# Optimization experiments

Measured on AMD Instinct MI355X. Metric: run time of the kernel, lower is better.

The kernel has to match this reference:

```python
import jax, jax.numpy as jnp
import numpy as np

HEADS, BS, HALO = 8, 8, 3
WIN = BS + 2 * HALO  # 14


def setup_inputs() -> dict:
    key = jax.random.key(0)
    k1, k2, k3, k4 = jax.random.split(key, 4)
    B, C, H, W = 16, 256, 64, 64
    dim_out_qk, dim_out_v = 256, 256
    std = C ** (-0.5)
    x = jax.random.normal(k1, (B, C, H, W), jnp.float32)
    Wq = jax.random.normal(k2, (dim_out_qk, C), jnp.float32) * std
    Wkv = jax.random.normal(k3, (dim_out_qk + dim_out_v, C), jnp.float32) * std
    pos_bias = jax.random.normal(k4, (HEADS, BS * BS, WIN * WIN), jnp.float32) * 0.02
    return {"x": x, "Wq": Wq, "Wkv": Wkv, "pos_bias": pos_bias}


def reference(x, Wq, Wkv, pos_bias):
    B, C, H, W = x.shape
    dhqk = Wq.shape[0] // HEADS            # 32
    dhv = Wkv.shape[0] // HEADS - dhqk     # 32
    scale = dhqk ** (-0.5)
    nhb, nwb = H // BS, W // BS
    nb = nhb * nwb

    xl = jnp.transpose(x, (0, 2, 3, 1))    # [B, H, W, C]

    # queries: [B, heads, nb, bs^2, dhqk] (row-major within block)
    q = xl @ Wq.T
    q = q.reshape(B, nhb, BS, nwb, BS, HEADS, dhqk)
    q = q.transpose(0, 5, 1, 3, 2, 4, 6).reshape(B, HEADS, nb, BS * BS, dhqk)

    # keys/values via overlapping halo windows (zero-padded unfold)
    kv = xl @ Wkv.T                                       # [B, H, W, dim_kv]
    kv = jnp.pad(kv, ((0, 0), (HALO, HALO), (HALO, HALO), (0, 0)))
    ridx = (jnp.arange(nhb) * BS)[:, None] + jnp.arange(WIN)[None, :]
    cidx = (jnp.arange(nwb) * BS)[:, None] + jnp.arange(WIN)[None, :]
    kv = kv[:, ridx]
    kv = kv[:, :, :, cidx]
    kv = kv.transpose(0, 1, 3, 2, 4, 5).reshape(B, nb, WIN * WIN, HEADS, dhqk + dhv)
    k = kv[..., :dhqk]
    v = kv[..., dhqk:]

    attn = jnp.einsum('bhnqd,bnkhd->bhnqk', q, k) * scale + pos_bias[None, :, None]
    attn = jax.nn.softmax(attn, axis=-1)
    out = jnp.einsum('bhnqk,bnkhd->bhnqd', attn, v)       # [B, heads, nb, bs^2, dhv]

    out = out.reshape(B, HEADS, nhb, nwb, BS, BS, dhv)
    out = out.transpose(0, 1, 6, 2, 4, 3, 5).reshape(B, HEADS * dhv, H, W)
    return out
```

## Files before the change

kernel.cpp:

```cpp
#include <hip/hip_runtime.h>
#include <hip/hip_bf16.h>
#include <stdint.h>

#define HEADS 8
#define WIN 14
#define NPOS 196
#define NPAD 224
#define NB 16
#define NC 256
#define NH 64
#define NW 64
#define NP 4096
#define NKV 512
#define NOC 768

typedef __bf16 bf16_t;
typedef bf16_t bf16x8 __attribute__((ext_vector_type(8)));
typedef float f32x4 __attribute__((ext_vector_type(4)));

union Frag {
  uint4 u4;
  bf16x8 b8;
  ushort us[8];
};

__device__ __forceinline__ ushort f2bf(float f) {
  bf16_t h = (bf16_t)f;
  return __builtin_bit_cast(ushort, h);
}
__device__ __forceinline__ bf16x8 load_bf8(const float* __restrict__ p) {
  float4 a = *reinterpret_cast<const float4*>(p);
  float4 b = *reinterpret_cast<const float4*>(p + 4);
  bf16x8 r;
  r[0] = (bf16_t)a.x; r[1] = (bf16_t)a.y; r[2] = (bf16_t)a.z; r[3] = (bf16_t)a.w;
  r[4] = (bf16_t)b.x; r[5] = (bf16_t)b.y; r[6] = (bf16_t)b.z; r[7] = (bf16_t)b.w;
  return r;
}

__device__ __forceinline__ void gload_lds16(const ushort* g, ushort* l) {
#if __has_builtin(__builtin_amdgcn_global_load_lds)
  __builtin_amdgcn_global_load_lds(
      (const __attribute__((address_space(1))) unsigned int*)(const void*)g,
      (__attribute__((address_space(3))) unsigned int*)(void*)l, 16, 0, 0);
#else
  *reinterpret_cast<uint4*>(l) = *reinterpret_cast<const uint4*>(g);
#endif
}

__device__ ushort g_wb[NOC * NC];
__device__ float g_pb2[HEADS * 4 * 14 * 256];

__global__ __launch_bounds__(256) void k_prep(const float* __restrict__ wq,
                                              const float* __restrict__ wkv,
                                              const float* __restrict__ pb) {
  const int wg = blockIdx.x;
  const int tid = threadIdx.x;
  if (wg < 96) {
    int idx = (wg * 256 + tid) * 8;
    int oc = idx >> 8, c = idx & 255;
    const float* src = (oc < 256) ? (wq + (size_t)oc * NC + c)
                                  : (wkv + (size_t)(oc - 256) * NC + c);
    Frag v;
    v.b8 = load_bf8(src);
    *reinterpret_cast<uint4*>(g_wb + idx) = v.u4;
  } else {
    int idx2 = wg - 96;
    int h = idx2 / 56;
    int rem = idx2 - h * 56;
    int w = rem / 14;
    int nt = rem - w * 14;
    int lane = tid >> 2, r = tid & 3;
    int quad = lane >> 4, lc = lane & 15;
    int q = w * 16 + lc;
    int key = nt * 16 + quad * 4 + r;
    float v = -100000.0f;
    if (key < NPOS)
      v = pb[((size_t)(h * 64 + q)) * NPOS + key] * 1.4426950408889634f;
    g_pb2[(size_t)idx2 * 256 + tid] = v;
  }
}

__global__ __launch_bounds__(256) void k_xt(const float* __restrict__ x,
                                            ushort* __restrict__ xt) {
  __shared__ __align__(16) ushort ls[64][66];
  const int b = blockIdx.z, p0 = blockIdx.x * 64, c0 = blockIdx.y * 64;
  const int by8 = blockIdx.y * 8;
  const int tid = threadIdx.x;
  #pragma unroll
  for (int it = 0; it < 4; ++it) {
    int i = it * 256 + tid;
    int c = i >> 4, ps = (i & 15) * 4;
    float4 v = *reinterpret_cast<const float4*>(x + ((size_t)(b * NC + c0 + c)) * NP + p0 + ps);
    ls[ps + 0][c] = f2bf(v.x);
    ls[ps + 1][c] = f2bf(v.y);
    ls[ps + 2][c] = f2bf(v.z);
    ls[ps + 3][c] = f2bf(v.w);
  }
  __syncthreads();
  #pragma unroll
  for (int it = 0; it < 2; ++it) {
    int i = it * 256 + tid;
    int p = i >> 3, gl = i & 7;
    Frag o;
    #pragma unroll
    for (int j = 0; j < 8; ++j) o.us[j] = ls[p][gl * 8 + j];
    int gph = by8 + (gl ^ (p & 7));
    *reinterpret_cast<uint4*>(xt + ((size_t)(b * NP) + p0 + p) * NC + gph * 8) = o.u4;
  }
}

__global__ __launch_bounds__(256, 2) void k_proj2(const ushort* __restrict__ xt,
                                                  ushort* __restrict__ qkv) {
  __shared__ __align__(16) ushort As[128 * 256];
  const int row0 = blockIdx.x * 128;
  const int n0 = blockIdx.y * 256;
  const int tid = threadIdx.x, lane = tid & 63, wid = tid >> 6;
  const int quad = lane >> 4, lc = lane & 15;
  const ushort* gs = xt + (size_t)row0 * NC;
  #pragma unroll
  for (int it = 0; it < 16; ++it) {
    int f = it * 256 + tid;
    gload_lds16(gs + (size_t)f * 8, As + f * 8);
  }
  __syncthreads();
  const int wm = (wid & 1) * 64, wn = (wid >> 1) * 128;
  f32x4 acc[4][8] = {};
  #pragma unroll
  for (int ks = 0; ks < 8; ++ks) {
    const int k0 = ks * 32 + quad * 8;
    Frag a[4];
    #pragma unroll
    for (int mt = 0; mt < 4; ++mt) {
      int row = wm + mt * 16 + lc;
      int gk = (ks * 4 + quad) ^ (lc & 7);
      a[mt].u4 = *reinterpret_cast<const uint4*>(&As[row * 256 + gk * 8]);
    }
    #pragma unroll
    for (int ng = 0; ng < 2; ++ng) {
      Frag bb[4];
      #pragma unroll
      for (int j = 0; j < 4; ++j) {
        int oc = n0 + wn + (ng * 4 + j) * 16 + lc;
        bb[j].u4 = *reinterpret_cast<const uint4*>(g_wb + (size_t)oc * NC + k0);
      }
      #pragma unroll
      for (int mt = 0; mt < 4; ++mt)
        #pragma unroll
        for (int j = 0; j < 4; ++j)
          acc[mt][ng * 4 + j] = __builtin_amdgcn_mfma_f32_16x16x32_bf16(
              a[mt].b8, bb[j].b8, acc[mt][ng * 4 + j], 0, 0, 0);
    }
  }
  __syncthreads();
  #pragma unroll
  for (int mt = 0; mt < 4; ++mt)
    #pragma unroll
    for (int nn = 0; nn < 8; ++nn) {
      int row = wm + mt * 16 + quad * 4;
      #pragma unroll
      for (int r = 0; r < 4; ++r) {
        int rr = row + r;
        int col = wn + nn * 16 + lc;
        As[rr * 256 + (((col >> 3) ^ (rr & 7)) * 8) + (col & 7)] = f2bf(acc[mt][nn][r]);
      }
    }
  __syncthreads();
  #pragma unroll
  for (int it = 0; it < 16; ++it) {
    int i = it * 256 + tid;
    int r = i >> 5, g = i & 31;
    uint4 u = *reinterpret_cast<const uint4*>(&As[r * 256 + ((g ^ (r & 7)) * 8)]);
    *reinterpret_cast<uint4*>(qkv + ((size_t)(row0 + r)) * NOC + n0 + g * 8) = u;
  }
}

__global__ __launch_bounds__(256) void k_attn_f2(const ushort* __restrict__ qkv,
                                                 float* __restrict__ out) {
  __shared__ __align__(16) ushort ksh[NPAD][40];
  __shared__ __align__(16) ushort vth[32][232];
  float (*osh)[33] = reinterpret_cast<float(*)[33]>(&ksh[0][0]);
  const int orig = blockIdx.x;
  const int wgid = (orig & 7) * 1024 + (orig >> 3);
  const int h = wgid & 7;
  const int blk = (wgid >> 3) & 63;
  const int b = wgid >> 9;
  const int by = blk >> 3, bx = blk & 7;
  const int tid = threadIdx.x, lane = tid & 63, w = tid >> 6;
  const int quad = lane >> 4, lc = lane & 15;

  Frag aq;
  {
    int q = w * 16 + lc;
    int py = by * 8 + (q >> 3), px = bx * 8 + (q & 7);
    aq.u4 = *reinterpret_cast<const uint4*>(
        qkv + ((size_t)(b * NP + py * NW + px)) * NOC + h * 32 + quad * 8);
  }

  #pragma unroll
  for (int it = 0; it < 7; ++it) {
    int i = it * 256 + tid;
    int pos = i >> 3, seg = i & 7;
    Frag v;
    v.u4 = make_uint4(0u, 0u, 0u, 0u);
    if (pos < NPOS) {
      int wy = pos / WIN;
      int wx = pos - wy * WIN;
      int yq = by * 8 - 3 + wy, xx = bx * 8 - 3 + wx;
      if ((unsigned)yq < (unsigned)NH && (unsigned)xx < (unsigned)NW)
        v.u4 = *reinterpret_cast<const uint4*>(
            qkv + ((size_t)(b * NP + yq * NW + xx)) * NOC + 256 + h * 64 + seg * 8);
    }
    if (seg < 4) {
      *reinterpret_cast<uint4*>(&ksh[pos][seg * 8]) = v.u4;
    } else {
      int d0 = (seg - 4) * 8;
      int cp = pos ^ ((seg - 4) << 3);
      #pragma unroll
      for (int j = 0; j < 8; ++j) vth[d0 + j][cp] = v.us[j];
    }
  }
  __syncthreads();

  f32x4 s[14];
  __builtin_amdgcn_s_setprio(1);
  #pragma unroll
  for (int nt = 0; nt < 14; ++nt) {
    Frag bk;
    bk.u4 = *reinterpret_cast<const uint4*>(&ksh[nt * 16 + lc][quad * 8]);
    f32x4 z = {0.f, 0.f, 0.f, 0.f};
    s[nt] = __builtin_amdgcn_mfma_f32_16x16x32_bf16(bk.b8, aq.b8, z, 0, 0, 0);
  }
  __builtin_amdgcn_s_setprio(0);

  const float ck = 0.17677669529663687f * 1.4426950408889634f;
  const float* __restrict__ pbw = g_pb2 + (size_t)((h * 4 + w) * 14) * 256;
  float lsum = 0.f;
  #pragma unroll
  for (int nt = 0; nt < 14; ++nt) {
    float4 bv4 = *reinterpret_cast<const float4*>(pbw + nt * 256 + lane * 4);
    #pragma unroll
    for (int r = 0; r < 4; ++r) {
      float p = exp2f(s[nt][r] * ck + (&bv4.x)[r]);
      s[nt][r] = p;
      lsum += p;
    }
  }

  f32x4 o[2] = {};
  #pragma unroll
  for (int kt = 0; kt < 7; ++kt) {
    Frag pa;
    #pragma unroll
    for (int j = 0; j < 8; ++j)
      pa.us[j] = f2bf(s[2 * kt + (j >> 2)][j & 3]);
    #pragma unroll
    for (int t = 0; t < 2; ++t) {
      int d = t * 16 + lc;
      int xr = ((d >> 3) & 3) << 3;
      int c0 = (kt * 32 + quad * 4) ^ xr;
      int c1 = (kt * 32 + 16 + quad * 4) ^ xr;
      Frag bv;
      *reinterpret_cast<uint2*>(&bv.us[0]) = *reinterpret_cast<const uint2*>(&vth[d][c0]);
      *reinterpret_cast<uint2*>(&bv.us[4]) = *reinterpret_cast<const uint2*>(&vth[d][c1]);
      o[t] = __builtin_amdgcn_mfma_f32_16x16x32_bf16(pa.b8, bv.b8, o[t], 0, 0, 0);
    }
  }

  lsum += __shfl_xor(lsum, 16);
  lsum += __shfl_xor(lsum, 32);
  float rl = 1.0f / lsum;
  float rinv[4];
  #pragma unroll
  for (int r = 0; r < 4; ++r)
    rinv[r] = __shfl(rl, (lane & 48) + quad * 4 + r);

  __syncthreads();
  #pragma unroll
  for (int t = 0; t < 2; ++t)
    #pragma unroll
    for (int r = 0; r < 4; ++r)
      osh[w * 16 + quad * 4 + r][t * 16 + lc] = o[t][r] * rinv[r];
  __syncthreads();

  {
    int d = tid >> 3, yy = tid & 7;
    float4 o0, o1;
    o0.x = osh[yy * 8 + 0][d]; o0.y = osh[yy * 8 + 1][d];
    o0.z = osh[yy * 8 + 2][d]; o0.w = osh[yy * 8 + 3][d];
    o1.x = osh[yy * 8 + 4][d]; o1.y = osh[yy * 8 + 5][d];
    o1.z = osh[yy * 8 + 6][d]; o1.w = osh[yy * 8 + 7][d];
    float* op = out + ((size_t)(b * NC + h * 32 + d) * NH + by * 8 + yy) * NW + bx * 8;
    *reinterpret_cast<float4*>(op) = o0;
    *reinterpret_cast<float4*>(op + 4) = o1;
  }
}

__global__ __launch_bounds__(256) void k_proj_r4(const float* __restrict__ x,
                                                 const float* __restrict__ wq,
                                                 const float* __restrict__ wkv,
                                                 ushort* __restrict__ qkv) {
  __shared__ __align__(16) ushort As[64][264];
  const int b = blockIdx.z, y = blockIdx.x;
  const int n0 = blockIdx.y * 256;
  const int tid = threadIdx.x, lane = tid & 63, wid = tid >> 6;
  const int quad = lane >> 4, lc = lane & 15;
  #pragma unroll
  for (int it = 0; it < 16; ++it) {
    int i = it * 256 + tid;
    int c = i >> 4, xs = (i & 15) * 4;
    float4 v = *reinterpret_cast<const float4*>(x + ((size_t)(b * NC + c)) * NP + y * NW + xs);
    #pragma unroll
    for (int j = 0; j < 4; ++j) {
      int row = xs + j;
      float f = (j == 0) ? v.x : (j == 1) ? v.y : (j == 2) ? v.z : v.w;
      As[row][c ^ ((((row >> 2) & 3)) << 3)] = f2bf(f);
    }
  }
  __syncthreads();
  const int wm = (wid & 1) * 32, wn = (wid >> 1) * 128;
  const int swz = ((lc >> 2) & 3) << 3;
  f32x4 acc[2][8] = {};
  #pragma unroll
  for (int ks = 0; ks < 8; ++ks) {
    const int k0 = ks * 32 + quad * 8;
    Frag a0, a1;
    a0.u4 = *reinterpret_cast<const uint4*>(&As[wm + lc][k0 ^ swz]);
    a1.u4 = *reinterpret_cast<const uint4*>(&As[wm + 16 + lc][k0 ^ swz]);
    #pragma unroll
    for (int nh = 0; nh < 2; ++nh) {
      bf16x8 bb[4];
      #pragma unroll
      for (int nt = 0; nt < 4; ++nt) {
        int oc = n0 + wn + nh * 64 + nt * 16 + lc;
        const float* wp = (oc < 256) ? (wq + (size_t)oc * NC) : (wkv + (size_t)(oc - 256) * NC);
        bb[nt] = load_bf8(wp + k0);
      }
      #pragma unroll
      for (int nt = 0; nt < 4; ++nt) {
        acc[0][nh * 4 + nt] = __builtin_amdgcn_mfma_f32_16x16x32_bf16(a0.b8, bb[nt], acc[0][nh * 4 + nt], 0, 0, 0);
        acc[1][nh * 4 + nt] = __builtin_amdgcn_mfma_f32_16x16x32_bf16(a1.b8, bb[nt], acc[1][nh * 4 + nt], 0, 0, 0);
      }
    }
  }
  __syncthreads();
  #pragma unroll
  for (int mt = 0; mt < 2; ++mt)
    #pragma unroll
    for (int nn = 0; nn < 8; ++nn)
      #pragma unroll
      for (int r = 0; r < 4; ++r)
        As[wm + mt * 16 + quad * 4 + r][wn + nn * 16 + lc] = f2bf(acc[mt][nn][r]);
  __syncthreads();
  #pragma unroll
  for (int v8 = 0; v8 < 8; ++v8) {
    int flat = v8 * 256 + tid;
    int p = flat >> 5, seg = flat & 31;
    uint4 u = *reinterpret_cast<const uint4*>(&As[p][seg * 8]);
    *reinterpret_cast<uint4*>(qkv + ((size_t)(b * NP) + y * NW + p) * NOC + n0 + seg * 8) = u;
  }
}

__global__ __launch_bounds__(256) void k_kv(const float* __restrict__ x,
                                            const float* __restrict__ wkv,
                                            ushort* __restrict__ kvb) {
  __shared__ __align__(16) ushort As[64][264];
  const int b = blockIdx.z;
  const int y = blockIdx.x;
  const int n0 = blockIdx.y * 128;
  const int tid = threadIdx.x;
  const int lane = tid & 63, wid = tid >> 6;
  const int quad = lane >> 4, lc = lane & 15;
  #pragma unroll
  for (int it = 0; it < 16; ++it) {
    int i = it * 256 + tid;
    int c = i >> 4, xs = (i & 15) * 4;
    float4 v = *reinterpret_cast<const float4*>(x + ((size_t)(b * NC + c)) * NP + y * NW + xs);
    As[xs + 0][c] = f2bf(v.x);
    As[xs + 1][c] = f2bf(v.y);
    As[xs + 2][c] = f2bf(v.z);
    As[xs + 3][c] = f2bf(v.w);
  }
  __syncthreads();
  const int wm = (wid & 1) * 32, wn = (wid >> 1) * 64;
  f32x4 acc[2][4] = {};
  #pragma unroll
  for (int ks = 0; ks < 8; ++ks) {
    const int k0 = ks * 32 + quad * 8;
    Frag a[2];
    bf16x8 bb[4];
    #pragma unroll
    for (int mt = 0; mt < 2; ++mt)
      a[mt].u4 = *reinterpret_cast<const uint4*>(&As[wm + mt * 16 + lc][k0]);
    #pragma unroll
    for (int nt = 0; nt < 4; ++nt) {
      int oc = n0 + wn + nt * 16 + lc;
      bb[nt] = load_bf8(wkv + (size_t)oc * NC + k0);
    }
    #pragma unroll
    for (int mt = 0; mt < 2; ++mt)
      #pragma unroll
      for (int nt = 0; nt < 4; ++nt)
        acc[mt][nt] = __builtin_amdgcn_mfma_f32_16x16x32_bf16(a[mt].b8, bb[nt], acc[mt][nt], 0, 0, 0);
  }
  #pragma unroll
  for (int mt = 0; mt < 2; ++mt) {
    #pragma unroll
    for (int r = 0; r < 4; ++r) {
      int pl = wm + mt * 16 + quad * 4 + r;
      #pragma unroll
      for (int nt = 0; nt < 4; ++nt) {
        int oc = n0 + wn + nt * 16 + lc;
        kvb[((size_t)(b * NP + y * NW + pl)) * NKV + oc] = f2bf(acc[mt][nt][r]);
      }
    }
  }
}

__global__ __launch_bounds__(256) void k_attn_v3(const float* __restrict__ x,
                                                 const float* __restrict__ wq,
                                                 const ushort* __restrict__ kvb,
                                                 const float* __restrict__ pbias,
                                                 float* __restrict__ out) {
  __shared__ __align__(16) ushort ksh[NPAD][40];
  __shared__ __align__(16) ushort vth[32][232];
  __shared__ __align__(16) ushort psh[4][16][232];
  __shared__ __align__(16) ushort qsh[4][16][32];
  __shared__ __align__(16) float osh[64][33];
  const int b = blockIdx.z, h = blockIdx.y, blk = blockIdx.x;
  const int by = blk >> 3, bx = blk & 7;
  const int tid = threadIdx.x, lane = tid & 63, w = tid >> 6;
  const int quad = lane >> 4, lc = lane & 15;

  for (int it = 0; it < 7; ++it) {
    int i = it * 256 + tid;
    int pos = i >> 3, seg = i & 7;
    Frag v;
    v.u4 = make_uint4(0u, 0u, 0u, 0u);
    if (pos < NPOS) {
      int wy = pos / WIN;
      int wx = pos - wy * WIN;
      int yq = by * 8 - 3 + wy, xx = bx * 8 - 3 + wx;
      if ((unsigned)yq < (unsigned)NH && (unsigned)xx < (unsigned)NW)
        v.u4 = *reinterpret_cast<const uint4*>(
            kvb + ((size_t)(b * NP + yq * NW + xx)) * NKV + h * 64 + seg * 8);
    }
    if (seg < 4) {
      *reinterpret_cast<uint4*>(&ksh[pos][seg * 8]) = v.u4;
    } else {
      int d0 = (seg - 4) * 8;
      #pragma unroll
      for (int j = 0; j < 8; ++j) vth[d0 + j][pos] = v.us[j];
    }
  }

  f32x4 qacc[2] = {};
  {
    const int q = w * 16 + lc;
    const size_t p = (size_t)(by * 8 + (q >> 3)) * NW + bx * 8 + (q & 7);
    #pragma unroll
    for (int ks = 0; ks < 8; ++ks) {
      const int k0 = ks * 32 + quad * 8;
      Frag ax;
      #pragma unroll
      for (int j = 0; j < 8; ++j)
        ax.us[j] = f2bf(x[((size_t)(b * NC + k0 + j)) * NP + p]);
      bf16x8 bw0 = load_bf8(wq + (size_t)(h * 32 + lc) * NC + k0);
      bf16x8 bw1 = load_bf8(wq + (size_t)(h * 32 + 16 + lc) * NC + k0);
      qacc[0] = __builtin_amdgcn_mfma_f32_16x16x32_bf16(ax.b8, bw0, qacc[0], 0, 0, 0);
      qacc[1] = __builtin_amdgcn_mfma_f32_16x16x32_bf16(ax.b8, bw1, qacc[1], 0, 0, 0);
    }
  }
  #pragma unroll
  for (int t = 0; t < 2; ++t)
    #pragma unroll
    for (int r = 0; r < 4; ++r)
      qsh[w][quad * 4 + r][t * 16 + lc] = f2bf(qacc[t][r]);
  Frag aq;
  aq.u4 = *reinterpret_cast<const uint4*>(&qsh[w][lc][quad * 8]);

  __syncthreads();

  f32x4 s[14];
  #pragma unroll
  for (int nt = 0; nt < 14; ++nt) {
    Frag bk;
    bk.u4 = *reinterpret_cast<const uint4*>(&ksh[nt * 16 + lc][quad * 8]);
    f32x4 z = {0.f, 0.f, 0.f, 0.f};
    s[nt] = __builtin_amdgcn_mfma_f32_16x16x32_bf16(aq.b8, bk.b8, z, 0, 0, 0);
  }

  const float scale = 0.17677669529663687f;
  const int qi = w * 16 + quad * 4;
  float lsum[4] = {0.f, 0.f, 0.f, 0.f};
  #pragma unroll
  for (int nt = 0; nt < 14; ++nt) {
    int col = nt * 16 + lc;
    #pragma unroll
    for (int r = 0; r < 4; ++r) {
      float p = 0.f;
      if (col < NPOS)
        p = __expf(s[nt][r] * scale + pbias[(size_t)(h * 64 + qi + r) * NPOS + col]);
      s[nt][r] = p;
      lsum[r] += p;
    }
  }
  #pragma unroll
  for (int m = 1; m < 16; m <<= 1) {
    #pragma unroll
    for (int r = 0; r < 4; ++r) lsum[r] += __shfl_xor(lsum[r], m);
  }
  #pragma unroll
  for (int nt = 0; nt < 14; ++nt) {
    #pragma unroll
    for (int r = 0; r < 4; ++r) psh[w][quad * 4 + r][nt * 16 + lc] = f2bf(s[nt][r]);
  }
  f32x4 o[2] = {};
  #pragma unroll
  for (int kt = 0; kt < 7; ++kt) {
    Frag ap;
    ap.u4 = *reinterpret_cast<const uint4*>(&psh[w][lc][kt * 32 + quad * 8]);
    #pragma unroll
    for (int t = 0; t < 2; ++t) {
      Frag bv;
      bv.u4 = *reinterpret_cast<const uint4*>(&vth[t * 16 + lc][kt * 32 + quad * 8]);
      o[t] = __builtin_amdgcn_mfma_f32_16x16x32_bf16(ap.b8, bv.b8, o[t], 0, 0, 0);
    }
  }
  #pragma unroll
  for (int t = 0; t < 2; ++t)
    #pragma unroll
    for (int r = 0; r < 4; ++r)
      osh[w * 16 + quad * 4 + r][t * 16 + lc] = o[t][r] / lsum[r];
  __syncthreads();
  {
    int d = tid >> 3, yy = tid & 7;
    float4 o0, o1;
    o0.x = osh[yy * 8 + 0][d]; o0.y = osh[yy * 8 + 1][d];
    o0.z = osh[yy * 8 + 2][d]; o0.w = osh[yy * 8 + 3][d];
    o1.x = osh[yy * 8 + 4][d]; o1.y = osh[yy * 8 + 5][d];
    o1.z = osh[yy * 8 + 6][d]; o1.w = osh[yy * 8 + 7][d];
    float* op = out + ((size_t)(b * NC + h * 32 + d) * NH + by * 8 + yy) * NW + bx * 8;
    *reinterpret_cast<float4*>(op) = o0;
    *reinterpret_cast<float4*>(op + 4) = o1;
  }
}

extern "C" void kernel_launch(void* const* d_in, const int* in_sizes, int n_in,
                              void* d_out, int out_size, void* d_ws, size_t ws_size,
                              hipStream_t stream) {
  const float* x   = (const float*)d_in[0];
  const float* wq  = (const float*)d_in[1];
  const float* wkv = (const float*)d_in[2];
  const float* pb  = (const float*)d_in[3];
  float* outp = (float*)d_out;

  const size_t qkv_bytes = (size_t)NB * NP * NOC * sizeof(ushort);
  const size_t xt_bytes  = (size_t)NB * NP * NC * sizeof(ushort);

  if (ws_size >= qkv_bytes + xt_bytes) {
    ushort* qkv = (ushort*)d_ws;
    ushort* xt  = (ushort*)((char*)d_ws + qkv_bytes);
    k_prep<<<dim3(544), 256, 0, stream>>>(wq, wkv, pb);
    k_xt<<<dim3(NP / 64, NC / 64, NB), 256, 0, stream>>>(x, xt);
    k_proj2<<<dim3(NB * NP / 128, 3), 256, 0, stream>>>(xt, qkv);
    k_attn_f2<<<dim3(NB * HEADS * 64), 256, 0, stream>>>(qkv, outp);
  } else if (ws_size >= qkv_bytes) {
    ushort* qkv = (ushort*)d_ws;
    k_prep<<<dim3(544), 256, 0, stream>>>(wq, wkv, pb);
    k_proj_r4<<<dim3(NH, 3, NB), 256, 0, stream>>>(x, wq, wkv, qkv);
    k_attn_f2<<<dim3(NB * HEADS * 64), 256, 0, stream>>>(qkv, outp);
  } else {
    ushort* kvb = (ushort*)d_ws;
    k_kv<<<dim3(NH, NKV / 128, NB), 256, 0, stream>>>(x, wkv, kvb);
    k_attn_v3<<<dim3(64, HEADS, NB), 256, 0, stream>>>(x, wq, kvb, pb, outp);
  }
}
```

Baseline: 289.0 us.

## Compute all QKV outputs per row tile and simplify halo window key layout

Measured after the change: 319.1 us. +10.4%, slower.

```diff
diff --git a/kernel.cpp b/kernel.cpp
--- a/kernel.cpp
+++ b/kernel.cpp
@@ -13,6 +13,7 @@
 #define NP 4096
 #define NKV 512
 #define NOC 768
+#define VSTR 228
 
 typedef __bf16 bf16_t;
 typedef bf16_t bf16x8 __attribute__((ext_vector_type(8)));
@@ -72,10 +73,11 @@
     int lane = tid >> 2, r = tid & 3;
     int quad = lane >> 4, lc = lane & 15;
     int q = w * 16 + lc;
-    int key = nt * 16 + quad * 4 + r;
+    int kp = nt * 16 + quad * 4 + r;
+    int wy = kp >> 4, wx = kp & 15;
     float v = -100000.0f;
-    if (key < NPOS)
-      v = pb[((size_t)(h * 64 + q)) * NPOS + key] * 1.4426950408889634f;
+    if (wx < WIN)
+      v = pb[((size_t)(h * 64 + q)) * NPOS + wy * WIN + wx] * 1.4426950408889634f;
     g_pb2[(size_t)idx2 * 256 + tid] = v;
   }
 }
@@ -111,73 +113,77 @@
 
 __global__ __launch_bounds__(256, 2) void k_proj2(const ushort* __restrict__ xt,
                                                   ushort* __restrict__ qkv) {
-  __shared__ __align__(16) ushort As[128 * 256];
-  const int row0 = blockIdx.x * 128;
-  const int n0 = blockIdx.y * 256;
+  __shared__ __align__(16) ushort As[64 * 256];
+  __shared__ __align__(16) ushort Ep[64 * 256];
+  const int row0 = blockIdx.x * 64;
   const int tid = threadIdx.x, lane = tid & 63, wid = tid >> 6;
   const int quad = lane >> 4, lc = lane & 15;
   const ushort* gs = xt + (size_t)row0 * NC;
   #pragma unroll
-  for (int it = 0; it < 16; ++it) {
+  for (int it = 0; it < 8; ++it) {
     int f = it * 256 + tid;
     gload_lds16(gs + (size_t)f * 8, As + f * 8);
   }
   __syncthreads();
-  const int wm = (wid & 1) * 64, wn = (wid >> 1) * 128;
-  f32x4 acc[4][8] = {};
-  #pragma unroll
-  for (int ks = 0; ks < 8; ++ks) {
-    const int k0 = ks * 32 + quad * 8;
-    Frag a[4];
-    #pragma unroll
-    for (int mt = 0; mt < 4; ++mt) {
-      int row = wm + mt * 16 + lc;
-      int gk = (ks * 4 + quad) ^ (lc & 7);
-      a[mt].u4 = *reinterpret_cast<const uint4*>(&As[row * 256 + gk * 8]);
-    }
-    #pragma unroll
-    for (int ng = 0; ng < 2; ++ng) {
-      Frag bb[4];
-      #pragma unroll
-      for (int j = 0; j < 4; ++j) {
-        int oc = n0 + wn + (ng * 4 + j) * 16 + lc;
-        bb[j].u4 = *reinterpret_cast<const uint4*>(g_wb + (size_t)oc * NC + k0);
+  const int wm = (wid & 1) * 32, wn = (wid >> 1) * 128;
+  #pragma unroll 1
+  for (int ny = 0; ny < 3; ++ny) {
+    const int n0 = ny * 256;
+    f32x4 acc[2][8] = {};
+    #pragma unroll
+    for (int ks = 0; ks < 8; ++ks) {
+      const int k0 = ks * 32 + quad * 8;
+      Frag a[2];
+      #pragma unroll
+      for (int mt = 0; mt < 2; ++mt) {
+        int row = wm + mt * 16 + lc;
+        int gk = (ks * 4 + quad) ^ (lc & 7);
+        a[mt].u4 = *reinterpret_cast<const uint4*>(&As[row * 256 + gk * 8]);
       }
       #pragma unroll
-      for (int mt = 0; mt < 4; ++mt)
+      for (int ng = 0; ng < 2; ++ng) {
+        Frag bb[4];
         #pragma unroll
-        for (int j = 0; j < 4; ++j)
-          acc[mt][ng * 4 + j] = __builtin_amdgcn_mfma_f32_16x16x32_bf16(
-              a[mt].b8, bb[j].b8, acc[mt][ng * 4 + j], 0, 0, 0);
-    }
-  }
-  __syncthreads();
-  #pragma unroll
-  for (int mt = 0; mt < 4; ++mt)
-    #pragma unroll
-    for (int nn = 0; nn < 8; ++nn) {
-      int row = wm + mt * 16 + quad * 4;
-      #pragma unroll
-      for (int r = 0; r < 4; ++r) {
-        int rr = row + r;
-        int col = wn + nn * 16 + lc;
-        As[rr * 256 + (((col >> 3) ^ (rr & 7)) * 8) + (col & 7)] = f2bf(acc[mt][nn][r]);
+        for (int j = 0; j < 4; ++j) {
+          int oc = n0 + wn + (ng * 4 + j) * 16 + lc;
+          bb[j].u4 = *reinterpret_cast<const uint4*>(g_wb + (size_t)oc * NC + k0);
+        }
+        #pragma unroll
+        for (int mt = 0; mt < 2; ++mt)
+          #pragma unroll
+          for (int j = 0; j < 4; ++j)
+            acc[mt][ng * 4 + j] = __builtin_amdgcn_mfma_f32_16x16x32_bf16(
+                a[mt].b8, bb[j].b8, acc[mt][ng * 4 + j], 0, 0, 0);
       }
     }
-  __syncthreads();
-  #pragma unroll
-  for (int it = 0; it < 16; ++it) {
-    int i = it * 256 + tid;
-    int r = i >> 5, g = i & 31;
-    uint4 u = *reinterpret_cast<const uint4*>(&As[r * 256 + ((g ^ (r & 7)) * 8)]);
-    *reinterpret_cast<uint4*>(qkv + ((size_t)(row0 + r)) * NOC + n0 + g * 8) = u;
+    #pragma unroll
+    for (int mt = 0; mt < 2; ++mt)
+      #pragma unroll
+      for (int nn = 0; nn < 8; ++nn) {
+        int rowb = wm + mt * 16 + quad * 4;
+        #pragma unroll
+        for (int r = 0; r < 4; ++r) {
+          int rr = rowb + r;
+          int col = wn + nn * 16 + lc;
+          Ep[rr * 256 + (((col >> 3) ^ (rr & 7)) * 8) + (col & 7)] = f2bf(acc[mt][nn][r]);
+        }
+      }
+    __syncthreads();
+    #pragma unroll
+    for (int it = 0; it < 8; ++it) {
+      int i = it * 256 + tid;
+      int r = i >> 5, g = i & 31;
+      uint4 u = *reinterpret_cast<const uint4*>(&Ep[r * 256 + ((g ^ (r & 7)) * 8)]);
+      *reinterpret_cast<uint4*>(qkv + ((size_t)(row0 + r)) * NOC + n0 + g * 8) = u;
+    }
+    __syncthreads();
   }
 }
 
 __global__ __launch_bounds__(256) void k_attn_f2(const ushort* __restrict__ qkv,
                                                  float* __restrict__ out) {
   __shared__ __align__(16) ushort ksh[NPAD][40];
-  __shared__ __align__(16) ushort vth[32][232];
+  __shared__ __align__(16) ushort vth[32 * VSTR];
   float (*osh)[33] = reinterpret_cast<float(*)[33]>(&ksh[0][0]);
   const int orig = blockIdx.x;
   const int wgid = (orig & 7) * 1024 + (orig >> 3);
@@ -200,23 +206,20 @@
   for (int it = 0; it < 7; ++it) {
     int i = it * 256 + tid;
     int pos = i >> 3, seg = i & 7;
+    int wy = pos >> 4, wx = pos & 15;
     Frag v;
     v.u4 = make_uint4(0u, 0u, 0u, 0u);
-    if (pos < NPOS) {
-      int wy = pos / WIN;
-      int wx = pos - wy * WIN;
-      int yq = by * 8 - 3 + wy, xx = bx * 8 - 3 + wx;
-      if ((unsigned)yq < (unsigned)NH && (unsigned)xx < (unsigned)NW)
-        v.u4 = *reinterpret_cast<const uint4*>(
-            qkv + ((size_t)(b * NP + yq * NW + xx)) * NOC + 256 + h * 64 + seg * 8);
-    }
+    int yq = by * 8 - 3 + wy, xx = bx * 8 - 3 + wx;
+    if (wx < WIN && (unsigned)yq < (unsigned)NH && (unsigned)xx < (unsigned)NW)
+      v.u4 = *reinterpret_cast<const uint4*>(
+          qkv + ((size_t)(b * NP + yq * NW + xx)) * NOC + 256 + h * 64 + seg * 8);
     if (seg < 4) {
       *reinterpret_cast<uint4*>(&ksh[pos][seg * 8]) = v.u4;
     } else {
       int d0 = (seg - 4) * 8;
       int cp = pos ^ ((seg - 4) << 3);
       #pragma unroll
-      for (int j = 0; j < 8; ++j) vth[d0 + j][cp] = v.us[j];
+      for (int j = 0; j < 8; ++j) vth[(d0 + j) * VSTR + cp] = v.us[j];
     }
   }
   __syncthreads();
@@ -260,8 +263,8 @@
       int c0 = (kt * 32 + quad * 4) ^ xr;
       int c1 = (kt * 32 + 16 + quad * 4) ^ xr;
       Frag bv;
-      *reinterpret_cast<uint2*>(&bv.us[0]) = *reinterpret_cast<const uint2*>(&vth[d][c0]);
-      *reinterpret_cast<uint2*>(&bv.us[4]) = *reinterpret_cast<const uint2*>(&vth[d][c1]);
+      *reinterpret_cast<uint2*>(&bv.us[0]) = *reinterpret_cast<const uint2*>(&vth[d * VSTR + c0]);
+      *reinterpret_cast<uint2*>(&bv.us[4]) = *reinterpret_cast<const uint2*>(&vth[d * VSTR + c1]);
       o[t] = __builtin_amdgcn_mfma_f32_16x16x32_bf16(pa.b8, bv.b8, o[t], 0, 0, 0);
     }
   }
@@ -562,7 +565,7 @@
     ushort* xt  = (ushort*)((char*)d_ws + qkv_bytes);
     k_prep<<<dim3(544), 256, 0, stream>>>(wq, wkv, pb);
     k_xt<<<dim3(NP / 64, NC / 64, NB), 256, 0, stream>>>(x, xt);
-    k_proj2<<<dim3(NB * NP / 128, 3), 256, 0, stream>>>(xt, qkv);
+    k_proj2<<<dim3(NB * NP / 64), 256, 0, stream>>>(xt, qkv);
     k_attn_f2<<<dim3(NB * HEADS * 64), 256, 0, stream>>>(qkv, outp);
   } else if (ws_size >= qkv_bytes) {
     ushort* qkv = (ushort*)d_ws;
```
